# Optimization experiments

Hardware: AMD Instinct MI355X
Metric: run time of the kernel (lower is better)

The kernel has to match this reference:

```python
import jax, jax.numpy as jnp
import numpy as np

T, B, N, L = 1024, 2, 10000, 30   # frames, batch(=2, hardcoded in original), vocab, glosses/sample
S = 2 * L + 1                      # blank-interleaved (CTC-extended) label length


def setup_inputs() -> dict:
    key = jax.random.key(0)
    k1, k2 = jax.random.split(key)
    logits = jax.random.normal(k1, (T, B, N), dtype=jnp.float32)
    label = jax.random.randint(k2, (B * L,), 1, N, dtype=jnp.int32)  # real glosses are >=1 (0 is blank)
    logits_len = jnp.full((B,), T, dtype=jnp.int32)
    label_len = jnp.full((B,), L, dtype=jnp.int32)
    return {"logits": logits, "logits_len": logits_len, "label": label, "label_len": label_len}


def _extend(lab):
    # [l1, l2, ...] -> [0, l1, 0, l2, ..., 0]  (blank-interleaved), shape (S,)
    return jnp.zeros((S,), lab.dtype).at[1::2].set(lab)


def _reach_fwd(ext):
    # map_forward[j, i] > 0  <=>  state j reachable from start at time i (CTC forward lattice).
    pad2 = jnp.full((2,), -1, ext.dtype)
    allow2 = (ext != 0) & (ext != jnp.concatenate([pad2, ext[:-2]]))  # skip-2 allowed
    init = jnp.zeros((S,), bool).at[0].set(True).at[1].set(True)

    def step(c, _):
        s1 = jnp.concatenate([jnp.zeros((1,), bool), c[:-1]])
        s2 = jnp.concatenate([jnp.zeros((2,), bool), c[:-2]]) & allow2
        n = c | s1 | s2
        return n, n

    _, outs = jax.lax.scan(step, init, None, length=T - 1)
    return jnp.concatenate([init[None], outs], axis=0)  # (T, S)


def _reach_bwd(ext):
    # map_backward[j, i] > 0  <=>  end reachable from state j at time i.
    pad2 = jnp.full((2,), -1, ext.dtype)
    allow2 = (ext != 0) & (ext != jnp.concatenate([ext[2:], pad2]))
    init = jnp.zeros((S,), bool).at[S - 1].set(True).at[S - 2].set(True)

    def step(c, _):
        s1 = jnp.concatenate([c[1:], jnp.zeros((1,), bool)])
        s2 = jnp.concatenate([c[2:], jnp.zeros((2,), bool)]) & allow2
        n = c | s1 | s2
        return n, n

    _, outs = jax.lax.scan(step, init, None, length=T - 1)
    return jnp.concatenate([outs[::-1], init[None]], axis=0)  # (T, S), time 0..T-1


def _forward(logits, label):
    labels = label.reshape(B, L)
    ext = jax.vmap(_extend)(labels)            # (B, S)
    rf = jax.vmap(_reach_fwd)(ext)             # (B, T, S)
    rb = jax.vmap(_reach_bwd)(ext)             # (B, T, S)
    sel = (rf & rb).astype(logits.dtype)       # map_final != 0 on the lattice

    def per_sample(logit, e, s):
        # mask[t, v] = any lattice state j with ext[j] == v active at time t
        mask = jnp.zeros((T, N), logit.dtype).at[:, e].max(s) > 0
        # original builds final_label as a detached numpy copy of logit at masked entries
        target = jax.lax.stop_gradient(jnp.where(mask, logit, jnp.zeros((), logit.dtype)))
        return jnp.sum((logit - target) ** 2)  # nn.MSELoss(reduction='sum')

    losses = jax.vmap(per_sample)(jnp.transpose(logits, (1, 0, 2)), ext, sel)
    return jnp.mean(losses)  # (loss1 + loss2) / 2


def reference(logits, logits_len, label, label_len):
    # logits_len / label_len are fixed to full lengths (T, L) so shapes stay static.
    return _forward(logits, label)
```

## Files before the change

kernel.cpp:

```cpp
#include <hip/hip_runtime.h>
#include <stdint.h>

typedef unsigned long long u64;

static constexpr int T = 1024;
static constexpr int B = 2;
static constexpr int N = 10000;
static constexpr int L = 30;
static constexpr int S = 2 * L + 1;

static constexpr int NBLK  = 2048;
static constexpr int CHUNK = 2500;
static constexpr int TAIL  = CHUNK - 9 * 256;

static constexpr u64 ALL   = (1ULL << S) - 1;
static constexpr u64 EVENM = 0x5555555555555555ULL & ((1ULL << S) - 1);

__device__ __forceinline__ float block_reduce(float s) {
    for (int off = 32; off; off >>= 1) s += __shfl_down(s, off, 64);
    __shared__ float tmp[8];
    int lane = threadIdx.x & 63, w = threadIdx.x >> 6;
    int nw = blockDim.x >> 6;
    if (lane == 0) tmp[w] = s;
    __syncthreads();
    float t = 0.f;
    if (threadIdx.x == 0)
        for (int i = 0; i < nw; ++i) t += tmp[i];
    return t;
}

__device__ __forceinline__ float sq4(float4 v) {
    return v.x * v.x + v.y * v.y + v.z * v.z + v.w * v.w;
}

__global__ void k_fused(const float4* __restrict__ x4, const float* __restrict__ x,
                        const int* __restrict__ label, float* __restrict__ partials) {
    float s = 0.f;
    int tid = threadIdx.x;

    if (blockIdx.x < 256) {
        __shared__ int labs[B][L];
        __shared__ u64 dups[B][L];
        __shared__ u64 AfS[B], AbS[B];
        if (tid < B) {
            int b = tid;
            int lb[L];
            u64 Af = 0, Ab = 0;
            #pragma unroll
            for (int k = 0; k < L; ++k) { lb[k] = label[b * L + k]; labs[b][k] = lb[k]; }
            #pragma unroll
            for (int k = 0; k < L; ++k) {
                u64 bit = 1ULL << (2 * k + 1);
                if (k == 0     || lb[k] != lb[k - 1]) Af |= bit;
                if (k == L - 1 || lb[k] != lb[k + 1]) Ab |= bit;
                u64 d = 0;
                for (int k2 = 0; k2 < k; ++k2)
                    if (lb[k2] == lb[k]) d |= 1ULL << (2 * k2 + 1);
                dups[b][k] = d;
            }
            AfS[b] = Af; AbS[b] = Ab;
        }
        __syncthreads();
        int pair = blockIdx.x * 8 + (tid >> 5);
        int lane = tid & 31;
        int b = pair >> 10;
        int t = pair & (T - 1);
        u64 m;
        if (t < 64) {
            u64 Af = AfS[b];
            u64 c = 3ULL;
            for (int i = 0; i < t; ++i) c = (c | (c << 1) | ((c << 2) & Af)) & ALL;
            m = c;
        } else if (t >= T - 64) {
            u64 Ab = AbS[b];
            u64 c = (1ULL << (S - 1)) | (1ULL << (S - 2));
            int n = T - 1 - t;
            for (int i = 0; i < n; ++i) c = c | (c >> 1) | ((c >> 2) & Ab);
            m = c;
        } else {
            m = ALL;
        }
        const float* row = x + (size_t)t * (B * N) + (size_t)b * N;
        if (lane < L) {
            u64 bit = 1ULL << (2 * lane + 1);
            if ((m & bit) && !(m & dups[b][lane])) {
                float v = row[labs[b][lane]];
                s -= v * v;
            }
        } else if (lane == L) {
            if (m & EVENM) { float v = row[0]; s -= v * v; }
        }
    }

    const float4* p = x4 + (size_t)blockIdx.x * CHUNK + tid;
    float4 v[5];
    #pragma unroll
    for (int j = 0; j < 5; ++j) v[j] = p[j * 256];
    #pragma unroll
    for (int j = 0; j < 5; ++j) s += sq4(v[j]);
    #pragma unroll
    for (int j = 0; j < 4; ++j) v[j] = p[(5 + j) * 256];
    v[4] = (tid < TAIL) ? p[9 * 256] : make_float4(0.f, 0.f, 0.f, 0.f);
    #pragma unroll
    for (int j = 0; j < 5; ++j) s += sq4(v[j]);

    float tot = block_reduce(s);
    if (threadIdx.x == 0) partials[blockIdx.x] = tot;
}

__global__ void k_final(const float* __restrict__ partials, float* __restrict__ out) {
    float s = 0.f;
    for (int i = threadIdx.x; i < NBLK; i += 256) s += partials[i];
    float tot = block_reduce(s);
    if (threadIdx.x == 0) out[0] = 0.5f * tot;
}

extern "C" void kernel_launch(void* const* d_in, const int* in_sizes, int n_in,
                              void* d_out, int out_size, void* d_ws, size_t ws_size,
                              hipStream_t stream) {
    const float* logits = (const float*)d_in[0];
    const int*   label  = (const int*)d_in[2];
    float* partials = (float*)d_ws;

    k_fused<<<NBLK, 256, 0, stream>>>((const float4*)logits, logits, label, partials);
    k_final<<<1, 256, 0, stream>>>(partials, (float*)d_out);
}
```

Measured before the change: 118.8 us.

## Fuse final reduction via last-block atomic counter and spread gather across all blocks

Removes the separate final-reduction kernel. Each block now publishes its partial sum and increments a global atomic counter, and the last block to arrive sums all partials. The per-row gather correction is spread so every block handles one (batch, time) row, instead of the first 256 blocks each handling 8 rows with a shared preprocessing step. The duplicate-label check is now computed per thread against the active mask rather than precomputed. This adds a memset launch for the counter, and the last-block reduction serialises the tail of the kernel.

```diff
diff --git a/kernel.cpp b/kernel.cpp
--- a/kernel.cpp
+++ b/kernel.cpp
@@ -34,45 +34,33 @@
 }
 
 __global__ void k_fused(const float4* __restrict__ x4, const float* __restrict__ x,
-                        const int* __restrict__ label, float* __restrict__ partials) {
+                        const int* __restrict__ label, float* __restrict__ partials,
+                        unsigned* __restrict__ counter, float* __restrict__ out) {
+    int tid = threadIdx.x;
     float s = 0.f;
-    int tid = threadIdx.x;
 
-    if (blockIdx.x < 256) {
-        __shared__ int labs[B][L];
-        __shared__ u64 dups[B][L];
-        __shared__ u64 AfS[B], AbS[B];
-        if (tid < B) {
-            int b = tid;
-            int lb[L];
-            u64 Af = 0, Ab = 0;
-            #pragma unroll
-            for (int k = 0; k < L; ++k) { lb[k] = label[b * L + k]; labs[b][k] = lb[k]; }
-            #pragma unroll
-            for (int k = 0; k < L; ++k) {
-                u64 bit = 1ULL << (2 * k + 1);
-                if (k == 0     || lb[k] != lb[k - 1]) Af |= bit;
-                if (k == L - 1 || lb[k] != lb[k + 1]) Ab |= bit;
-                u64 d = 0;
-                for (int k2 = 0; k2 < k; ++k2)
-                    if (lb[k2] == lb[k]) d |= 1ULL << (2 * k2 + 1);
-                dups[b][k] = d;
-            }
-            AfS[b] = Af; AbS[b] = Ab;
-        }
-        __syncthreads();
-        int pair = blockIdx.x * 8 + (tid >> 5);
-        int lane = tid & 31;
-        int b = pair >> 10;
-        int t = pair & (T - 1);
+    const int b = blockIdx.x >> 10;
+    const int t = blockIdx.x & (T - 1);
+
+    __shared__ int labs[L];
+    if (tid < L) labs[tid] = label[b * L + tid];
+    __syncthreads();
+
+    if (tid < 32) {
         u64 m;
         if (t < 64) {
-            u64 Af = AfS[b];
+            u64 Af = 0;
+            #pragma unroll
+            for (int k = 0; k < L; ++k)
+                if (k == 0 || labs[k] != labs[k - 1]) Af |= 1ULL << (2 * k + 1);
             u64 c = 3ULL;
             for (int i = 0; i < t; ++i) c = (c | (c << 1) | ((c << 2) & Af)) & ALL;
             m = c;
         } else if (t >= T - 64) {
-            u64 Ab = AbS[b];
+            u64 Ab = 0;
+            #pragma unroll
+            for (int k = 0; k < L; ++k)
+                if (k == L - 1 || labs[k] != labs[k + 1]) Ab |= 1ULL << (2 * k + 1);
             u64 c = (1ULL << (S - 1)) | (1ULL << (S - 2));
             int n = T - 1 - t;
             for (int i = 0; i < n; ++i) c = c | (c >> 1) | ((c >> 2) & Ab);
@@ -81,14 +69,17 @@
             m = ALL;
         }
         const float* row = x + (size_t)t * (B * N) + (size_t)b * N;
-        if (lane < L) {
-            u64 bit = 1ULL << (2 * lane + 1);
-            if ((m & bit) && !(m & dups[b][lane])) {
-                float v = row[labs[b][lane]];
-                s -= v * v;
+        if (tid < L) {
+            u64 bit = 1ULL << (2 * tid + 1);
+            if (m & bit) {
+                int v = labs[tid];
+                bool dup = false;
+                for (int k2 = 0; k2 < tid; ++k2)
+                    if (labs[k2] == v && (m & (1ULL << (2 * k2 + 1)))) { dup = true; break; }
+                if (!dup) { float xv = row[v]; s -= xv * xv; }
             }
-        } else if (lane == L) {
-            if (m & EVENM) { float v = row[0]; s -= v * v; }
+        } else if (tid == L) {
+            if (m & EVENM) { float xv = row[0]; s -= xv * xv; }
         }
     }
 
@@ -105,14 +96,22 @@
     for (int j = 0; j < 5; ++j) s += sq4(v[j]);
 
     float tot = block_reduce(s);
-    if (threadIdx.x == 0) partials[blockIdx.x] = tot;
-}
 
-__global__ void k_final(const float* __restrict__ partials, float* __restrict__ out) {
-    float s = 0.f;
-    for (int i = threadIdx.x; i < NBLK; i += 256) s += partials[i];
-    float tot = block_reduce(s);
-    if (threadIdx.x == 0) out[0] = 0.5f * tot;
+    __shared__ bool isLast;
+    if (tid == 0) {
+        partials[blockIdx.x] = tot;
+        __threadfence();
+        unsigned old = atomicAdd(counter, 1u);
+        isLast = (old == NBLK - 1);
+    }
+    __syncthreads();
+    if (isLast) {
+        __threadfence();
+        float s2 = 0.f;
+        for (int i = tid; i < NBLK; i += 256) s2 += partials[i];
+        float t2 = block_reduce(s2);
+        if (tid == 0) out[0] = 0.5f * t2;
+    }
 }
 
 extern "C" void kernel_launch(void* const* d_in, const int* in_sizes, int n_in,
@@ -120,8 +119,10 @@
                               hipStream_t stream) {
     const float* logits = (const float*)d_in[0];
     const int*   label  = (const int*)d_in[2];
-    float* partials = (float*)d_ws;
+    float*    partials = (float*)d_ws;
+    unsigned* counter  = (unsigned*)((char*)d_ws + 8192);
 
-    k_fused<<<NBLK, 256, 0, stream>>>((const float4*)logits, logits, label, partials);
-    k_final<<<1, 256, 0, stream>>>(partials, (float*)d_out);
+    hipMemsetAsync(counter, 0, 4, stream);
+    k_fused<<<NBLK, 256, 0, stream>>>((const float4*)logits, logits, label,
+                                      partials, counter, (float*)d_out);
 }
```

Result: slower. 202.8 us (+70.7%).
